# Performance work log

Measured on AMD Instinct MI355X. Metric: run time of the kernel, lower is better.

The kernel has to match this reference:

```python
import jax, jax.numpy as jnp
import numpy as np

N = 100000      # nodes
E = 1600000     # edges (avg degree 16)
D_IN, D_H, D_OUT = 128, 128, 40
BN_EPS = 1e-5


def _gcn_norm(edge_index):
    # add self-loops, compute symmetric normalization D^-1/2 (A+I) D^-1/2
    loops = jnp.arange(N, dtype=edge_index.dtype)
    src = jnp.concatenate([edge_index[0], loops])
    dst = jnp.concatenate([edge_index[1], loops])
    deg = jax.ops.segment_sum(jnp.ones(src.shape[0], jnp.float32), dst, num_segments=N)
    dinv = jnp.where(deg > 0, jax.lax.rsqrt(deg), 0.0)
    norm = dinv[src] * dinv[dst]  # [E+N]
    return src, dst, norm


def _gcn_conv(h, W, b, src, dst, norm):
    h = h @ W                          # [N, d_out]
    msg = h[src] * norm[:, None]       # [E+N, d_out] gather + scale
    out = jax.ops.segment_sum(msg, dst, num_segments=N)
    return out + b


def _bn(h, g, beta, mean, var):
    return g * (h - mean) * jax.lax.rsqrt(var + BN_EPS) + beta


def setup_inputs() -> dict:
    key = jax.random.key(0)
    ks = jax.random.split(key, 16)
    x = jax.random.normal(ks[0], (N, D_IN), jnp.float32)
    edge_index = jax.random.randint(ks[1], (2, E), 0, N, dtype=jnp.int32)
    s_in, s_h = 1.0 / np.sqrt(D_IN), 1.0 / np.sqrt(D_H)
    W0 = jax.random.normal(ks[2], (D_IN, D_H), jnp.float32) * s_in
    b0 = jnp.zeros((D_H,), jnp.float32)
    W1 = jax.random.normal(ks[3], (D_H, D_H), jnp.float32) * s_h
    b1 = jnp.zeros((D_H,), jnp.float32)
    W2 = jax.random.normal(ks[4], (D_H, D_OUT), jnp.float32) * s_h
    b2 = jnp.zeros((D_OUT,), jnp.float32)
    g0 = jnp.ones((D_H,), jnp.float32)
    be0 = jnp.zeros((D_H,), jnp.float32)
    m0 = jax.random.normal(ks[5], (D_H,), jnp.float32) * 0.1
    v0 = jax.random.uniform(ks[6], (D_H,), jnp.float32) + 0.5
    g1 = jnp.ones((D_H,), jnp.float32)
    be1 = jnp.zeros((D_H,), jnp.float32)
    m1 = jax.random.normal(ks[7], (D_H,), jnp.float32) * 0.1
    v1 = jax.random.uniform(ks[8], (D_H,), jnp.float32) + 0.5
    return {"x": x, "edge_index": edge_index,
            "W0": W0, "b0": b0, "W1": W1, "b1": b1, "W2": W2, "b2": b2,
            "g0": g0, "be0": be0, "m0": m0, "v0": v0,
            "g1": g1, "be1": be1, "m1": m1, "v1": v1}


def reference(x, edge_index, W0, b0, W1, b1, W2, b2,
              g0, be0, m0, v0, g1, be1, m1, v1):
    src, dst, norm = _gcn_norm(edge_index)
    h = _gcn_conv(x, W0, b0, src, dst, norm)
    h = jax.nn.relu(_bn(h, g0, be0, m0, v0))   # dropout = identity in eval
    h = _gcn_conv(h, W1, b1, src, dst, norm)
    h = jax.nn.relu(_bn(h, g1, be1, m1, v1))
    h = _gcn_conv(h, W2, b2, src, dst, norm)
    return jax.nn.log_softmax(h, axis=1)
```

## Files before the change

### kernel.cpp

```cpp
#include <hip/hip_runtime.h>
#include <math.h>


#define CSHIFT 9
#define CSZ 512
#define PCHUNK 8192

typedef unsigned short u16;
typedef unsigned int u32;
typedef unsigned char u8;
typedef float f32x4 __attribute__((ext_vector_type(4)));
typedef short s16x8 __attribute__((ext_vector_type(8)));

__device__ inline float bflo(u32 u) { return __uint_as_float(u << 16); }
__device__ inline float bfhi(u32 u) { return __uint_as_float(u & 0xffff0000u); }
__device__ inline u16 f2bf(float f) {
    u32 b = __float_as_uint(f);
    b += 0x7fff + ((b >> 16) & 1);
    return (u16)(b >> 16);
}
__device__ inline u32 pack2(float lo, float hi) {
    return (u32)f2bf(lo) | ((u32)f2bf(hi) << 16);
}


__global__ __launch_bounds__(256) void k_hist1(const int* __restrict__ dst,
                                               int* __restrict__ hist1,
                                               int E, int NB) {
    __shared__ int h[256];
    int t = threadIdx.x;
    h[t] = 0;
    __syncthreads();
    for (int i = blockIdx.x * 256 * 16 + t; i < min(E, (blockIdx.x + 1) * 256 * 16);
         i += 256)
        atomicAdd(&h[dst[i] >> CSHIFT], 1);
    __syncthreads();
    if (t < NB && h[t]) atomicAdd(&hist1[t], h[t]);
}

__global__ __launch_bounds__(256) void k_scan1(const int* __restrict__ hist1,
                                               int* __restrict__ base1,
                                               int* __restrict__ cur1,
                                               int NB, int E) {
    __shared__ int sc[256];
    int t = threadIdx.x;
    int v = (t < NB) ? hist1[t] : 0;
    sc[t] = v;
    __syncthreads();
    for (int d = 1; d < 256; d <<= 1) {
        int add = (t >= d) ? sc[t - d] : 0;
        __syncthreads();
        sc[t] += add;
        __syncthreads();
    }
    if (t < NB) {
        int excl = sc[t] - v;
        base1[t] = excl;
        cur1[t] = excl;
    }
    if (t == 0) base1[NB] = E;
}

__global__ __launch_bounds__(256) void k_part1(const int* __restrict__ src,
                                               const int* __restrict__ dst,
                                               int* __restrict__ cur1,
                                               u32* __restrict__ bkt,
                                               int E, int NB) {
    __shared__ u32 stage[PCHUNK];
    __shared__ u8 sbin[PCHUNK];
    __shared__ int cnt[256];
    __shared__ int lbase[256];
    __shared__ int lcur[256];
    __shared__ int gb[256];
    int t = threadIdx.x;
    int base = blockIdx.x * PCHUNK;
    int n = min(PCHUNK, E - base);
    cnt[t] = 0;
    __syncthreads();
    for (int i = t; i < n; i += 256) atomicAdd(&cnt[dst[base + i] >> CSHIFT], 1);
    __syncthreads();
    int v = cnt[t];
    lbase[t] = v;
    __syncthreads();
    for (int d = 1; d < 256; d <<= 1) {
        int add = (t >= d) ? lbase[t - d] : 0;
        __syncthreads();
        lbase[t] += add;
        __syncthreads();
    }
    {
        int excl = lbase[t] - v;
        __syncthreads();
        lbase[t] = excl;
        lcur[t] = excl;
        if (t < NB && v) gb[t] = atomicAdd(&cur1[t], v);
    }
    __syncthreads();
    for (int i = t; i < n; i += 256) {
        int d = dst[base + i];
        int s = src[base + i];
        int bin = d >> CSHIFT;
        int p = atomicAdd(&lcur[bin], 1);
        stage[p] = ((u32)s << CSHIFT) | (u32)(d & (CSZ - 1));
        sbin[p] = (u8)bin;
    }
    __syncthreads();
    for (int k = t; k < n; k += 256) {
        int bin = sbin[k];
        bkt[gb[bin] + (k - lbase[bin])] = stage[k];
    }
}

__global__ __launch_bounds__(256) void k_csr(const u32* __restrict__ bkt,
                                             const int* __restrict__ base1,
                                             int* __restrict__ col,
                                             int* __restrict__ row,
                                             float* __restrict__ dinv,
                                             int N, int E) {
    __shared__ int deg[CSZ];
    __shared__ int cur[CSZ];
    __shared__ int sc[256];
    int b = blockIdx.x;
    int t = threadIdx.x;
    int start = base1[b];
    int end = base1[b + 1];
    int nbase = b << CSHIFT;
    deg[t] = 0;
    deg[t + 256] = 0;
    __syncthreads();
    for (int i = start + t; i < end; i += 256)
        atomicAdd(&deg[bkt[i] & (CSZ - 1)], 1);
    __syncthreads();
    int d0 = deg[2 * t], d1 = deg[2 * t + 1];
    int s = d0 + d1;
    sc[t] = s;
    __syncthreads();
    for (int d = 1; d < 256; d <<= 1) {
        int add = (t >= d) ? sc[t - d] : 0;
        __syncthreads();
        sc[t] += add;
        __syncthreads();
    }
    int excl = sc[t] - s;
    cur[2 * t] = excl;
    cur[2 * t + 1] = excl + d0;
    int n0 = nbase + 2 * t, n1 = n0 + 1;
    if (n0 < N) { row[n0] = start + excl;      dinv[n0] = rsqrtf((float)(d0 + 1)); }
    if (n1 < N) { row[n1] = start + excl + d0; dinv[n1] = rsqrtf((float)(d1 + 1)); }
    __syncthreads();
    for (int i = start + t; i < end; i += 256) {
        u32 v = bkt[i];
        int p = start + atomicAdd(&cur[v & (CSZ - 1)], 1);
        col[p] = (int)(v >> CSHIFT);
    }
    if (b == 0 && t == 0) row[N] = E;
}


__global__ __launch_bounds__(256) void k_packW(const float* __restrict__ W,
                                               u16* __restrict__ Wpk) {
    int g = blockIdx.x * 256 + threadIdx.x;
    int j = g & 7;
    int l = (g >> 3) & 63;
    int f = g >> 9;
    int ct = f & 7, ks = f >> 3;
    int krow = ks * 32 + ((l >> 4) << 3) + j;
    int wcol = ct * 16 + (l & 15);
    Wpk[g] = f2bf(W[krow * 128 + wcol]);
}

__global__ __launch_bounds__(256) void k_packW40(const float* __restrict__ W,
                                                 u16* __restrict__ Wpk) {
    int g = blockIdx.x * 256 + threadIdx.x;
    if (g >= 12 * 512) return;
    int j = g & 7;
    int l = (g >> 3) & 63;
    int f = g >> 9;
    int ct = f % 3, ks = f / 3;
    int krow = ks * 32 + ((l >> 4) << 3) + j;
    int wcol = ct * 16 + (l & 15);
    Wpk[g] = (wcol < 40) ? f2bf(W[krow * 40 + wcol]) : (u16)0;
}


__global__ __launch_bounds__(256) void k_gemm0(const float* __restrict__ A,
                                               const u16* __restrict__ Wpk,
                                               u16* __restrict__ C,
                                               const float* __restrict__ dinv,
                                               int M) {
    int tid = threadIdx.x;
    int wv = blockIdx.x * 4 + (tid >> 6);
    int rowbase = wv * 16;
    if (rowbase >= M) return;
    int l = tid & 63;
    int r = l & 15, hi = l >> 4;

    f32x4 acc[8];
#pragma unroll
    for (int ct = 0; ct < 8; ++ct) acc[ct] = (f32x4)(0.f);

    const uint4* wp = (const uint4*)Wpk;
#pragma unroll
    for (int ks = 0; ks < 4; ++ks) {
        int abase = (min(rowbase + r, M - 1)) * 128 + ks * 32 + hi * 8;
        float4 a0 = *(const float4*)&A[abase];
        float4 a1 = *(const float4*)&A[abase + 4];
        uint4 u = make_uint4(pack2(a0.x, a0.y), pack2(a0.z, a0.w),
                             pack2(a1.x, a1.y), pack2(a1.z, a1.w));
        s16x8 afrag = *(s16x8*)&u;
#pragma unroll
        for (int ct = 0; ct < 8; ++ct) {
            uint4 b = wp[(ks * 8 + ct) * 64 + l];
            s16x8 bfrag = *(s16x8*)&b;
            acc[ct] = __builtin_amdgcn_mfma_f32_16x16x32_bf16(afrag, bfrag, acc[ct], 0, 0, 0);
        }
    }
    float dv[4];
#pragma unroll
    for (int reg = 0; reg < 4; ++reg) {
        int orow = rowbase + 4 * hi + reg;
        dv[reg] = (orow < M) ? dinv[orow] : 0.f;
    }
#pragma unroll
    for (int ct = 0; ct < 8; ++ct) {
#pragma unroll
        for (int reg = 0; reg < 4; ++reg) {
            int orow = rowbase + 4 * hi + reg;
            if (orow < M)
                C[(size_t)orow * 128 + ct * 16 + r] = f2bf(dv[reg] * acc[ct][reg]);
        }
    }
}


template <int NCT>
__global__ __launch_bounds__(512) void k_fused(const u16* __restrict__ X,
                                               const u16* __restrict__ Wpk,
                                               u16* __restrict__ O,
                                               const int* __restrict__ row,
                                               const int* __restrict__ col,
                                               const float* __restrict__ dinv,
                                               const float* __restrict__ bias,
                                               const float* __restrict__ g,
                                               const float* __restrict__ be,
                                               const float* __restrict__ mean,
                                               const float* __restrict__ var,
                                               int n, int ostride) {
    __shared__ u32 hl[16][64];
    int tid = threadIdx.x;
    int nl = tid >> 5;
    int l5 = tid & 31;
    int node = blockIdx.x * 16 + nl;
    int nc = min(node, n - 1);
    const uint2* xp = (const uint2*)X;
    int s = row[nc], e = row[nc + 1];

    uint2 v = xp[(size_t)nc * 32 + l5];
    float a0 = bflo(v.x), a1 = bfhi(v.x), a2 = bflo(v.y), a3 = bfhi(v.y);
    float b0 = 0, b1 = 0, b2 = 0, b3 = 0;
    float c0 = 0, c1 = 0, c2 = 0, c3 = 0;
    float d0 = 0, d1 = 0, d2 = 0, d3 = 0;
    int j = s;
    for (; j + 8 <= e; j += 8) {
        int e0 = col[j], e1 = col[j+1], e2 = col[j+2], e3 = col[j+3];
        int e4 = col[j+4], e5 = col[j+5], e6 = col[j+6], e7 = col[j+7];
        uint2 x0 = xp[(size_t)e0 * 32 + l5];
        uint2 x1 = xp[(size_t)e1 * 32 + l5];
        uint2 x2 = xp[(size_t)e2 * 32 + l5];
        uint2 x3 = xp[(size_t)e3 * 32 + l5];
        uint2 x4 = xp[(size_t)e4 * 32 + l5];
        uint2 x5 = xp[(size_t)e5 * 32 + l5];
        uint2 x6 = xp[(size_t)e6 * 32 + l5];
        uint2 x7 = xp[(size_t)e7 * 32 + l5];
        a0 += bflo(x0.x); a1 += bfhi(x0.x); a2 += bflo(x0.y); a3 += bfhi(x0.y);
        b0 += bflo(x1.x); b1 += bfhi(x1.x); b2 += bflo(x1.y); b3 += bfhi(x1.y);
        c0 += bflo(x2.x); c1 += bfhi(x2.x); c2 += bflo(x2.y); c3 += bfhi(x2.y);
        d0 += bflo(x3.x); d1 += bfhi(x3.x); d2 += bflo(x3.y); d3 += bfhi(x3.y);
        a0 += bflo(x4.x); a1 += bfhi(x4.x); a2 += bflo(x4.y); a3 += bfhi(x4.y);
        b0 += bflo(x5.x); b1 += bfhi(x5.x); b2 += bflo(x5.y); b3 += bfhi(x5.y);
        c0 += bflo(x6.x); c1 += bfhi(x6.x); c2 += bflo(x6.y); c3 += bfhi(x6.y);
        d0 += bflo(x7.x); d1 += bfhi(x7.x); d2 += bflo(x7.y); d3 += bfhi(x7.y);
    }
    for (; j + 2 <= e; j += 2) {
        int e0 = col[j], e1 = col[j+1];
        uint2 x0 = xp[(size_t)e0 * 32 + l5];
        uint2 x1 = xp[(size_t)e1 * 32 + l5];
        a0 += bflo(x0.x); a1 += bfhi(x0.x); a2 += bflo(x0.y); a3 += bfhi(x0.y);
        b0 += bflo(x1.x); b1 += bfhi(x1.x); b2 += bflo(x1.y); b3 += bfhi(x1.y);
    }
    if (j < e) {
        uint2 x0 = xp[(size_t)col[j] * 32 + l5];
        c0 += bflo(x0.x); c1 += bfhi(x0.x); c2 += bflo(x0.y); c3 += bfhi(x0.y);
    }
    float dvn = dinv[nc];
    float s0 = dvn * ((a0 + b0) + (c0 + d0));
    float s1 = dvn * ((a1 + b1) + (c1 + d1));
    float s2 = dvn * ((a2 + b2) + (c2 + d2));
    float s3 = dvn * ((a3 + b3) + (c3 + d3));
    float4 g4 = ((const float4*)g)[l5];
    float4 be4 = ((const float4*)be)[l5];
    float4 m4 = ((const float4*)mean)[l5];
    float4 v4 = ((const float4*)var)[l5];
    float4 bi4 = ((const float4*)bias)[l5];
    float sc0 = g4.x * rsqrtf(v4.x + 1e-5f);
    float sc1 = g4.y * rsqrtf(v4.y + 1e-5f);
    float sc2 = g4.z * rsqrtf(v4.z + 1e-5f);
    float sc3 = g4.w * rsqrtf(v4.w + 1e-5f);
    float y0 = fmaxf(fmaf(sc0, s0, fmaf(sc0, bi4.x - m4.x, be4.x)), 0.f);
    float y1 = fmaxf(fmaf(sc1, s1, fmaf(sc1, bi4.y - m4.y, be4.y)), 0.f);
    float y2 = fmaxf(fmaf(sc2, s2, fmaf(sc2, bi4.z - m4.z, be4.z)), 0.f);
    float y3 = fmaxf(fmaf(sc3, s3, fmaf(sc3, bi4.w - m4.w, be4.w)), 0.f);
    {
        int unit = (l5 >> 1) ^ nl;
        uint2* p = (uint2*)&hl[nl][(unit << 2) + ((l5 & 1) << 1)];
        *p = make_uint2(pack2(y0, y1), pack2(y2, y3));
    }
    __syncthreads();

    int w = tid >> 6;
    if (w < NCT) {
        int l = tid & 63;
        int r = l & 15, hi = l >> 4;
        f32x4 acc = (f32x4)(0.f);
        const uint4* wp = (const uint4*)Wpk;
#pragma unroll
        for (int ks = 0; ks < 4; ++ks) {
            int unit = (ks * 4 + hi) ^ r;
            uint4 a = *(const uint4*)&hl[r][unit << 2];
            s16x8 afrag = *(s16x8*)&a;
            uint4 b = wp[(ks * NCT + w) * 64 + l];
            s16x8 bfrag = *(s16x8*)&b;
            acc = __builtin_amdgcn_mfma_f32_16x16x32_bf16(afrag, bfrag, acc, 0, 0, 0);
        }
        int nbase = blockIdx.x * 16;
#pragma unroll
        for (int reg = 0; reg < 4; ++reg) {
            int orow = nbase + 4 * hi + reg;
            int oc = w * 16 + r;
            if (orow < n && (NCT == 8 || oc < 40))
                O[(size_t)orow * ostride + oc] = f2bf(dinv[orow] * acc[reg]);
        }
    }
}


__global__ __launch_bounds__(256) void k_agg40(const u16* __restrict__ X,
                                               float* __restrict__ out,
                                               const int* __restrict__ row,
                                               const int* __restrict__ col,
                                               const float* __restrict__ dinv,
                                               const float* __restrict__ b2,
                                               int n) {
    int tid = threadIdx.x;
    int wid = tid >> 6, lane = tid & 63;
    int half = lane >> 5, l5 = lane & 31;
    int node = (blockIdx.x * 4 + wid) * 2 + half;
    bool valid = node < n;
    int nc = valid ? node : (n - 1);
    bool active = l5 < 20;
    const u32* xp = (const u32*)X;
    int s = row[nc], e = row[nc + 1];
    int li = min(l5, 19);
    float a0 = 0, a1 = 0, b0 = 0, b1 = 0, c0 = 0, c1 = 0, d0 = 0, d1 = 0;
    {
        u32 v = xp[(size_t)nc * 20 + li];
        a0 = bflo(v); a1 = bfhi(v);
    }
    int j = s;
    for (; j + 8 <= e; j += 8) {
        int e0 = col[j], e1 = col[j+1], e2 = col[j+2], e3 = col[j+3];
        int e4 = col[j+4], e5 = col[j+5], e6 = col[j+6], e7 = col[j+7];
        u32 x0 = xp[(size_t)e0 * 20 + li];
        u32 x1 = xp[(size_t)e1 * 20 + li];
        u32 x2 = xp[(size_t)e2 * 20 + li];
        u32 x3 = xp[(size_t)e3 * 20 + li];
        u32 x4 = xp[(size_t)e4 * 20 + li];
        u32 x5 = xp[(size_t)e5 * 20 + li];
        u32 x6 = xp[(size_t)e6 * 20 + li];
        u32 x7 = xp[(size_t)e7 * 20 + li];
        a0 += bflo(x0); a1 += bfhi(x0);
        b0 += bflo(x1); b1 += bfhi(x1);
        c0 += bflo(x2); c1 += bfhi(x2);
        d0 += bflo(x3); d1 += bfhi(x3);
        a0 += bflo(x4); a1 += bfhi(x4);
        b0 += bflo(x5); b1 += bfhi(x5);
        c0 += bflo(x6); c1 += bfhi(x6);
        d0 += bflo(x7); d1 += bfhi(x7);
    }
    for (; j + 2 <= e; j += 2) {
        int e0 = col[j], e1 = col[j+1];
        u32 x0 = xp[(size_t)e0 * 20 + li];
        u32 x1 = xp[(size_t)e1 * 20 + li];
        a0 += bflo(x0); a1 += bfhi(x0);
        b0 += bflo(x1); b1 += bfhi(x1);
    }
    if (j < e) {
        u32 x0 = xp[(size_t)col[j] * 20 + li];
        c0 += bflo(x0); c1 += bfhi(x0);
    }
    float dv = dinv[nc];
    float ylo = -INFINITY, yhi = -INFINITY;
    if (active) {
        float2 bb = ((const float2*)b2)[l5];
        ylo = fmaf(dv, (a0 + b0) + (c0 + d0), bb.x);
        yhi = fmaf(dv, (a1 + b1) + (c1 + d1), bb.y);
    }
    float m = fmaxf(ylo, yhi);
#pragma unroll
    for (int d = 16; d; d >>= 1) m = fmaxf(m, __shfl_xor(m, d));
    float ex = active ? (__expf(ylo - m) + __expf(yhi - m)) : 0.f;
#pragma unroll
    for (int d = 16; d; d >>= 1) ex += __shfl_xor(ex, d);
    if (valid && active) {
        float lse = m + __logf(ex);
        ((float2*)out)[(size_t)node * 20 + l5] = make_float2(ylo - lse, yhi - lse);
    }
}


extern "C" void kernel_launch(void* const* d_in, const int* in_sizes, int n_in,
                              void* d_out, int out_size, void* d_ws, size_t ws_size,
                              hipStream_t stream) {
    const float* x   = (const float*)d_in[0];
    const int*   ei  = (const int*)d_in[1];
    const float* W0  = (const float*)d_in[2];
    const float* b0  = (const float*)d_in[3];
    const float* W1  = (const float*)d_in[4];
    const float* b1  = (const float*)d_in[5];
    const float* W2  = (const float*)d_in[6];
    const float* b2  = (const float*)d_in[7];
    const float* g0  = (const float*)d_in[8];
    const float* be0 = (const float*)d_in[9];
    const float* m0  = (const float*)d_in[10];
    const float* v0  = (const float*)d_in[11];
    const float* g1  = (const float*)d_in[12];
    const float* be1 = (const float*)d_in[13];
    const float* m1  = (const float*)d_in[14];
    const float* v1  = (const float*)d_in[15];
    float* out = (float*)d_out;

    int N = in_sizes[0] / 128;
    int E = in_sizes[1] / 2;
    const int* src = ei;
    const int* dst = ei + E;

    int NB = (N + CSZ - 1) / CSZ;

    char* ws = (char*)d_ws;
    size_t off = 0;
    auto alloc = [&](size_t bytes) -> char* {
        char* p = ws + off;
        off += (bytes + 255) & ~(size_t)255;
        return p;
    };
    u16*   XsA   = (u16*)alloc((size_t)N * 128 * 2);
    u16*   XsB   = (u16*)alloc((size_t)N * 128 * 2);
    u16*   bufC  = (u16*)alloc((size_t)N * 40 * 2);
    int*   col   = (int*)alloc((size_t)E * 4 + 64);
    int*   row   = (int*)alloc((size_t)(N + 1) * 4);
    float* dinv  = (float*)alloc((size_t)N * 4);
    int*   hist1 = (int*)alloc((size_t)(NB + 1) * 4);
    int*   base1 = (int*)alloc((size_t)(NB + 1) * 4);
    int*   cur1  = (int*)alloc((size_t)(NB + 1) * 4);
    u16*   Wpk0  = (u16*)alloc(128 * 128 * 2);
    u16*   Wpk1  = (u16*)alloc(128 * 128 * 2);
    u16*   Wpk2  = (u16*)alloc(128 * 48 * 2);
    u32*   bkt   = (u32*)XsA;

    hipMemsetAsync(hist1, 0, (size_t)(NB + 1) * 4, stream);
    k_hist1<<<(E + 4095) / 4096, 256, 0, stream>>>(dst, hist1, E, NB);
    k_scan1<<<1, 256, 0, stream>>>(hist1, base1, cur1, NB, E);
    k_part1<<<(E + PCHUNK - 1) / PCHUNK, 256, 0, stream>>>(src, dst, cur1, bkt, E, NB);
    k_csr<<<NB, 256, 0, stream>>>(bkt, base1, col, row, dinv, N, E);
    k_packW<<<64, 256, 0, stream>>>(W0, Wpk0);
    k_packW<<<64, 256, 0, stream>>>(W1, Wpk1);
    k_packW40<<<24, 256, 0, stream>>>(W2, Wpk2);

    int gemmGrid = ((N + 15) / 16 + 3) / 4;
    k_gemm0<<<gemmGrid, 256, 0, stream>>>(x, Wpk0, XsA, dinv, N);
    int fusedGrid = (N + 15) / 16;
    k_fused<8><<<fusedGrid, 512, 0, stream>>>(XsA, Wpk1, XsB, row, col, dinv,
                                              b0, g0, be0, m0, v0, N, 128);
    k_fused<3><<<fusedGrid, 512, 0, stream>>>(XsB, Wpk2, bufC, row, col, dinv,
                                              b1, g1, be1, m1, v1, N, 40);
    k_agg40<<<(N + 7) / 8, 256, 0, stream>>>(bufC, out, row, col, dinv, b2, N);
}
```

Baseline: 284.8 us.

## Make fused GCN layer wave-local, widen CSR block, halve partition chunk

The fused aggregate+GEMM kernel now has each 64-lane wave aggregate two nodes and run its own MFMAs over all output column tiles using wave-private shared memory. This removes the block-wide __syncthreads between aggregation and GEMM. In exchange, each MFMA uses only 2 of its 16 rows, so matrix work and weight loads rise about eightfold. Separately, the CSR build uses 1024-thread blocks with a single 512-entry scan, the partition chunk is halved to create more blocks, and the gemm0 epilogue reads dinv directly instead of precomputing it.

New measurement: 311.2 us. 1.09x slower.

```diff
diff --git a/kernel.cpp b/kernel.cpp
--- a/kernel.cpp
+++ b/kernel.cpp
@@ -4,7 +4,7 @@
 
 #define CSHIFT 9
 #define CSZ 512
-#define PCHUNK 8192
+#define PCHUNK 4096
 
 typedef unsigned short u16;
 typedef unsigned int u32;
@@ -111,47 +111,46 @@
     }
 }
 
-__global__ __launch_bounds__(256) void k_csr(const u32* __restrict__ bkt,
-                                             const int* __restrict__ base1,
-                                             int* __restrict__ col,
-                                             int* __restrict__ row,
-                                             float* __restrict__ dinv,
-                                             int N, int E) {
+__global__ __launch_bounds__(1024) void k_csr(const u32* __restrict__ bkt,
+                                              const int* __restrict__ base1,
+                                              int* __restrict__ col,
+                                              int* __restrict__ row,
+                                              float* __restrict__ dinv,
+                                              int N, int E) {
     __shared__ int deg[CSZ];
     __shared__ int cur[CSZ];
-    __shared__ int sc[256];
     int b = blockIdx.x;
     int t = threadIdx.x;
     int start = base1[b];
     int end = base1[b + 1];
-    int nbase = b << CSHIFT;
-    deg[t] = 0;
-    deg[t + 256] = 0;
-    __syncthreads();
-    for (int i = start + t; i < end; i += 256)
+    if (t < CSZ) deg[t] = 0;
+    __syncthreads();
+    for (int i = start + t; i < end; i += 1024)
         atomicAdd(&deg[bkt[i] & (CSZ - 1)], 1);
     __syncthreads();
-    int d0 = deg[2 * t], d1 = deg[2 * t + 1];
-    int s = d0 + d1;
-    sc[t] = s;
-    __syncthreads();
-    for (int d = 1; d < 256; d <<= 1) {
-        int add = (t >= d) ? sc[t - d] : 0;
-        __syncthreads();
-        sc[t] += add;
-        __syncthreads();
-    }
-    int excl = sc[t] - s;
-    cur[2 * t] = excl;
-    cur[2 * t + 1] = excl + d0;
-    int n0 = nbase + 2 * t, n1 = n0 + 1;
-    if (n0 < N) { row[n0] = start + excl;      dinv[n0] = rsqrtf((float)(d0 + 1)); }
-    if (n1 < N) { row[n1] = start + excl + d0; dinv[n1] = rsqrtf((float)(d1 + 1)); }
-    __syncthreads();
-    for (int i = start + t; i < end; i += 256) {
-        u32 v = bkt[i];
-        int p = start + atomicAdd(&cur[v & (CSZ - 1)], 1);
-        col[p] = (int)(v >> CSHIFT);
+    int v = (t < CSZ) ? deg[t] : 0;
+    if (t < CSZ) cur[t] = v;
+    __syncthreads();
+    for (int d = 1; d < CSZ; d <<= 1) {
+        int add = (t < CSZ && t >= d) ? cur[t - d] : 0;
+        __syncthreads();
+        if (t < CSZ) cur[t] += add;
+        __syncthreads();
+    }
+    if (t < CSZ) {
+        int excl = cur[t] - v;
+        int node = (b << CSHIFT) + t;
+        if (node < N) {
+            row[node] = start + excl;
+            dinv[node] = rsqrtf((float)(v + 1));
+        }
+        cur[t] = excl;
+    }
+    __syncthreads();
+    for (int i = start + t; i < end; i += 1024) {
+        u32 e = bkt[i];
+        int p = start + atomicAdd(&cur[e & (CSZ - 1)], 1);
+        col[p] = (int)(e >> CSHIFT);
     }
     if (b == 0 && t == 0) row[N] = E;
 }
@@ -215,26 +214,20 @@
             acc[ct] = __builtin_amdgcn_mfma_f32_16x16x32_bf16(afrag, bfrag, acc[ct], 0, 0, 0);
         }
     }
-    float dv[4];
-#pragma unroll
-    for (int reg = 0; reg < 4; ++reg) {
-        int orow = rowbase + 4 * hi + reg;
-        dv[reg] = (orow < M) ? dinv[orow] : 0.f;
-    }
 #pragma unroll
     for (int ct = 0; ct < 8; ++ct) {
 #pragma unroll
         for (int reg = 0; reg < 4; ++reg) {
             int orow = rowbase + 4 * hi + reg;
             if (orow < M)
-                C[(size_t)orow * 128 + ct * 16 + r] = f2bf(dv[reg] * acc[ct][reg]);
+                C[(size_t)orow * 128 + ct * 16 + r] = f2bf(dinv[orow] * acc[ct][reg]);
         }
     }
 }
 
 
 template <int NCT>
-__global__ __launch_bounds__(512) void k_fused(const u16* __restrict__ X,
+__global__ __launch_bounds__(256) void k_fused(const u16* __restrict__ X,
                                                const u16* __restrict__ Wpk,
                                                u16* __restrict__ O,
                                                const int* __restrict__ row,
@@ -246,11 +239,11 @@
                                                const float* __restrict__ mean,
                                                const float* __restrict__ var,
                                                int n, int ostride) {
-    __shared__ u32 hl[16][64];
+    __shared__ u32 hl[4][2][64];
     int tid = threadIdx.x;
-    int nl = tid >> 5;
-    int l5 = tid & 31;
-    int node = blockIdx.x * 16 + nl;
+    int wid = tid >> 6, lane = tid & 63;
+    int half = lane >> 5, l5 = lane & 31;
+    int node = (blockIdx.x * 4 + wid) * 2 + half;
     int nc = min(node, n - 1);
     const uint2* xp = (const uint2*)X;
     int s = row[nc], e = row[nc + 1];
@@ -310,35 +303,34 @@
     float y1 = fmaxf(fmaf(sc1, s1, fmaf(sc1, bi4.y - m4.y, be4.y)), 0.f);
     float y2 = fmaxf(fmaf(sc2, s2, fmaf(sc2, bi4.z - m4.z, be4.z)), 0.f);
     float y3 = fmaxf(fmaf(sc3, s3, fmaf(sc3, bi4.w - m4.w, be4.w)), 0.f);
-    {
-        int unit = (l5 >> 1) ^ nl;
-        uint2* p = (uint2*)&hl[nl][(unit << 2) + ((l5 & 1) << 1)];
-        *p = make_uint2(pack2(y0, y1), pack2(y2, y3));
-    }
-    __syncthreads();
-
-    int w = tid >> 6;
-    if (w < NCT) {
-        int l = tid & 63;
-        int r = l & 15, hi = l >> 4;
+
+    *(uint2*)&hl[wid][half][l5 * 2] = make_uint2(pack2(y0, y1), pack2(y2, y3));
+
+    int l = lane;
+    int r1 = l & 1, hi = l >> 4;
+    int node0 = (blockIdx.x * 4 + wid) * 2;
+    int node1 = node0 + 1;
+    float dv0 = dinv[min(node0, n - 1)];
+    float dv1 = dinv[min(node1, n - 1)];
+    const uint4* wp = (const uint4*)Wpk;
+    const u32* hw = &hl[wid][0][0];
+#pragma unroll
+    for (int ct = 0; ct < NCT; ++ct) {
         f32x4 acc = (f32x4)(0.f);
-        const uint4* wp = (const uint4*)Wpk;
 #pragma unroll
         for (int ks = 0; ks < 4; ++ks) {
-            int unit = (ks * 4 + hi) ^ r;
-            uint4 a = *(const uint4*)&hl[r][unit << 2];
+            uint4 a = *(const uint4*)&hw[r1 * 64 + ks * 16 + hi * 4];
             s16x8 afrag = *(s16x8*)&a;
-            uint4 b = wp[(ks * NCT + w) * 64 + l];
+            uint4 b = wp[(ks * NCT + ct) * 64 + l];
             s16x8 bfrag = *(s16x8*)&b;
             acc = __builtin_amdgcn_mfma_f32_16x16x32_bf16(afrag, bfrag, acc, 0, 0, 0);
         }
-        int nbase = blockIdx.x * 16;
-#pragma unroll
-        for (int reg = 0; reg < 4; ++reg) {
-            int orow = nbase + 4 * hi + reg;
-            int oc = w * 16 + r;
-            if (orow < n && (NCT == 8 || oc < 40))
-                O[(size_t)orow * ostride + oc] = f2bf(dinv[orow] * acc[reg]);
+        if (l < 16) {
+            int oc = ct * 16 + l;
+            if (NCT == 8 || oc < 40) {
+                if (node0 < n) O[(size_t)node0 * ostride + oc] = f2bf(dv0 * acc[0]);
+                if (node1 < n) O[(size_t)node1 * ostride + oc] = f2bf(dv1 * acc[1]);
+            }
         }
     }
 }
@@ -471,17 +463,17 @@
     k_hist1<<<(E + 4095) / 4096, 256, 0, stream>>>(dst, hist1, E, NB);
     k_scan1<<<1, 256, 0, stream>>>(hist1, base1, cur1, NB, E);
     k_part1<<<(E + PCHUNK - 1) / PCHUNK, 256, 0, stream>>>(src, dst, cur1, bkt, E, NB);
-    k_csr<<<NB, 256, 0, stream>>>(bkt, base1, col, row, dinv, N, E);
+    k_csr<<<NB, 1024, 0, stream>>>(bkt, base1, col, row, dinv, N, E);
     k_packW<<<64, 256, 0, stream>>>(W0, Wpk0);
     k_packW<<<64, 256, 0, stream>>>(W1, Wpk1);
     k_packW40<<<24, 256, 0, stream>>>(W2, Wpk2);
 
     int gemmGrid = ((N + 15) / 16 + 3) / 4;
     k_gemm0<<<gemmGrid, 256, 0, stream>>>(x, Wpk0, XsA, dinv, N);
-    int fusedGrid = (N + 15) / 16;
-    k_fused<8><<<fusedGrid, 512, 0, stream>>>(XsA, Wpk1, XsB, row, col, dinv,
+    int fusedGrid = (N + 7) / 8;
+    k_fused<8><<<fusedGrid, 256, 0, stream>>>(XsA, Wpk1, XsB, row, col, dinv,
                                               b0, g0, be0, m0, v0, N, 128);
-    k_fused<3><<<fusedGrid, 512, 0, stream>>>(XsB, Wpk2, bufC, row, col, dinv,
+    k_fused<3><<<fusedGrid, 256, 0, stream>>>(XsB, Wpk2, bufC, row, col, dinv,
                                               b1, g1, be1, m1, v1, N, 40);
     k_agg40<<<(N + 7) / 8, 256, 0, stream>>>(bufC, out, row, col, dinv, b2, N);
 }
```
